# Optimization experiments

Hardware: AMD Instinct MI355X
Metric: run time of the kernel (lower is better)

Reference implementation:

```python
import jax, jax.numpy as jnp
import numpy as np

B, T, D, H, O = 64, 2048, 256, 256, 256


def setup_inputs() -> dict:
    key = jax.random.key(0)
    ks = jax.random.split(key, 4)
    s_d = float(1.0 / np.sqrt(D))
    s_h = float(1.0 / np.sqrt(H))
    return {
        "x": jax.random.normal(ks[0], (B, T, D), jnp.float32),
        "c0": jnp.zeros((B, H), jnp.float32),
        "h0": jnp.zeros((B, H), jnp.float32),
        "Wih": jax.random.normal(ks[1], (D, 4 * H), jnp.float32) * s_d,
        "Whh": jax.random.normal(ks[2], (H, 4 * H), jnp.float32) * s_h,
        "bh": jnp.zeros((4 * H,), jnp.float32),
        "Wout": jax.random.normal(ks[3], (H, O), jnp.float32) * s_h,
        "bout": jnp.zeros((O,), jnp.float32),
    }


def reference(x, c0, h0, Wih, Whh, bh, Wout, bout):
    # Teacher-forcing OneToManyRNN: LSTM cell + Dense projection each step.
    # Gate order (flax LSTMCell): i, f, g, o.
    def step(carry, xt):
        c, h = carry
        gates = xt @ Wih + h @ Whh + bh  # [B, 4H]
        i, f, g, o = jnp.split(gates, 4, axis=-1)
        i = jax.nn.sigmoid(i)
        f = jax.nn.sigmoid(f)
        g = jnp.tanh(g)
        o = jax.nn.sigmoid(o)
        c_new = f * c + i * g
        h_new = o * jnp.tanh(c_new)
        y = h_new @ Wout + bout  # dense_out projection
        return (c_new, h_new), y

    xs = jnp.swapaxes(x, 0, 1)  # [T, B, D]
    _, ys = jax.lax.scan(step, (c0, h0), xs)
    return jnp.swapaxes(ys, 0, 1)  # [B, T, O] (stacked per-step outputs)
```

## Files before the change

kernel.cpp:

```cpp
#include <hip/hip_runtime.h>
#include <hip/hip_fp16.h>
#include <cstdint>
#include <cstddef>

typedef _Float16 half_t;
typedef _Float16 half2_t __attribute__((ext_vector_type(2)));
typedef _Float16 half8_t __attribute__((ext_vector_type(8)));
typedef float    f32x4   __attribute__((ext_vector_type(4)));

#define T_FULL  2048
#define T_CH    512
#define N_CHUNK 4
#define B_SZ    64
#define H_SZ    256
#define G4      1024
#define CH_M    (B_SZ * T_CH)

#define KP_RF   48
#define KP_LDS  7
#define KP_STR  9

static constexpr size_t OFF_XW   = 0;
static constexpr size_t OFF_H    = OFF_XW   + (size_t)CH_M * G4 * 2;
static constexpr size_t OFF_WIH  = OFF_H    + (size_t)CH_M * H_SZ * 2;
static constexpr size_t OFF_WOUT = OFF_WIH  + (size_t)G4 * 256 * 2;
static constexpr size_t OFF_WRF  = OFF_WOUT + (size_t)256 * 256 * 2;
static constexpr size_t OFF_WLDS = OFF_WRF  + (size_t)2 * KP_RF * 1024 * 4;
static constexpr size_t OFF_WSTR = OFF_WLDS + (size_t)2 * KP_LDS * 256 * 16;
static constexpr size_t OFF_SC   = OFF_WSTR + (size_t)2 * KP_STR * 256 * 16;
static constexpr size_t OFF_SH   = OFF_SC   + (size_t)B_SZ * H_SZ * 4;

__device__ __forceinline__ unsigned int packh2(float a, float b) {
    half2_t h; h.x = (half_t)a; h.y = (half_t)b;
    return __builtin_bit_cast(unsigned int, h);
}

__device__ __forceinline__ float dot2f(unsigned int hp, unsigned int wp, float acc) {
#if __has_builtin(__builtin_amdgcn_fdot2)
    return __builtin_amdgcn_fdot2(__builtin_bit_cast(half2_t, hp),
                                  __builtin_bit_cast(half2_t, wp), acc, false);
#else
    half2_t h = __builtin_bit_cast(half2_t, hp);
    half2_t w = __builtin_bit_cast(half2_t, wp);
    return fmaf((float)h.y, (float)w.y, fmaf((float)h.x, (float)w.x, acc));
#endif
}

__device__ __forceinline__ unsigned int rlane(unsigned int v, int lane) {
    return (unsigned int)__builtin_amdgcn_readlane((int)v, lane);
}

__device__ __forceinline__ float sigm(float x)  { return 1.0f / (1.0f + __expf(-x)); }
__device__ __forceinline__ float tanh_(float x) { return 1.0f - 2.0f / (__expf(2.0f * x) + 1.0f); }

static constexpr int PACK_TOTAL = 262144 + 65536 + 2 * KP_RF * 1024
                                + 2 * KP_LDS * 256 * 4 + 2 * KP_STR * 256 * 4
                                + 16384 + 8192;

__global__ __launch_bounds__(256) void pack_kernel(
    const float* __restrict__ Wih, const float* __restrict__ Whh,
    const float* __restrict__ Wout, const float* __restrict__ c0,
    const float* __restrict__ h0,
    half_t* __restrict__ wih_t, half_t* __restrict__ wout_t,
    unsigned int* __restrict__ whh_rf, unsigned int* __restrict__ whh_lds,
    unsigned int* __restrict__ whh_str,
    float* __restrict__ state_c, unsigned int* __restrict__ state_h)
{
    const int stride = gridDim.x * blockDim.x;
    for (int idx = blockIdx.x * blockDim.x + threadIdx.x; idx < PACK_TOTAL; idx += stride) {
        int r = idx;
        if (r < 262144) {
            int n = r >> 8, k = r & 255;
            wih_t[r] = (half_t)Wih[k * 1024 + n];
            continue;
        }
        r -= 262144;
        if (r < 65536) {
            int n = r >> 8, k = r & 255;
            wout_t[r] = (half_t)Wout[k * 256 + n];
            continue;
        }
        r -= 65536;
        if (r < 2 * KP_RF * 1024) {
            int col = r & 1023, q2 = r >> 10;
            int hh = q2 / KP_RF, pl = q2 % KP_RF;
            int k0 = 2 * (hh * 64 + pl);
            whh_rf[r] = packh2(Whh[k0 * 1024 + col], Whh[(k0 + 1) * 1024 + col]);
            continue;
        }
        r -= 2 * KP_RF * 1024;
        if (r < 2 * KP_LDS * 256 * 4) {
            int j = r & 3, e = (r >> 2) & 255, rest = r >> 10;
            int ql = rest % KP_LDS, hh = rest / KP_LDS;
            int k0 = 2 * (hh * 64 + KP_RF + ql);
            int col = j * 256 + e;
            whh_lds[r] = packh2(Whh[k0 * 1024 + col], Whh[(k0 + 1) * 1024 + col]);
            continue;
        }
        r -= 2 * KP_LDS * 256 * 4;
        if (r < 2 * KP_STR * 256 * 4) {
            int j = r & 3, e = (r >> 2) & 255, rest = r >> 10;
            int sl = rest % KP_STR, hh = rest / KP_STR;
            int k0 = 2 * (hh * 64 + KP_RF + KP_LDS + sl);
            int col = j * 256 + e;
            whh_str[r] = packh2(Whh[k0 * 1024 + col], Whh[(k0 + 1) * 1024 + col]);
            continue;
        }
        r -= 2 * KP_STR * 256 * 4;
        if (r < 16384) { state_c[r] = c0[r]; continue; }
        r -= 16384;
        state_h[r] = packh2(h0[2 * r], h0[2 * r + 1]);
    }
}

template<int AMODE, int CMODE>
__global__ __launch_bounds__(256) void gemm16(
    const void* __restrict__ Ap, const half_t* __restrict__ Bt,
    void* __restrict__ Cp, const float* __restrict__ bias, int chunk0)
{
    __shared__ half_t Als[128][40];
    __shared__ half_t Bls[128][40];
    const int tid  = threadIdx.x;
    const int lane = tid & 63, wid = tid >> 6;
    const int wr = wid >> 1, wc = wid & 1;
    const int m0 = blockIdx.x * 128, n0 = blockIdx.y * 128;

    f32x4 acc[4][4] = {};

    for (int kc = 0; kc < 8; ++kc) {
        __syncthreads();
        if (AMODE == 1) {
            const float* A = (const float*)Ap;
            #pragma unroll
            for (int i = 0; i < 4; ++i) {
                int l = tid + i * 256;
                int row = l >> 3, kq = l & 7;
                int m = m0 + row;
                int arow = ((m >> 9) << 11) + chunk0 + (m & 511);
                f32x4 v = *(const f32x4*)(A + (size_t)arow * 256 + kc * 32 + kq * 4);
                uint2 pk;
                pk.x = packh2(v.x, v.y);
                pk.y = packh2(v.z, v.w);
                *reinterpret_cast<uint2*>(&Als[row][kq * 4]) = pk;
            }
        } else {
            const half_t* A = (const half_t*)Ap;
            #pragma unroll
            for (int i = 0; i < 2; ++i) {
                int l = tid + i * 256;
                int row = l >> 2, ko = l & 3;
                half8_t v = *(const half8_t*)(A + (size_t)(m0 + row) * 256 + kc * 32 + ko * 8);
                *reinterpret_cast<half8_t*>(&Als[row][ko * 8]) = v;
            }
        }
        #pragma unroll
        for (int i = 0; i < 2; ++i) {
            int l = tid + i * 256;
            int row = l >> 2, ko = l & 3;
            half8_t v = *(const half8_t*)(Bt + (size_t)(n0 + row) * 256 + kc * 32 + ko * 8);
            *reinterpret_cast<half8_t*>(&Bls[row][ko * 8]) = v;
        }
        __syncthreads();

        half8_t af[4], bf[4];
        #pragma unroll
        for (int mi = 0; mi < 4; ++mi)
            af[mi] = *reinterpret_cast<const half8_t*>(&Als[wr * 64 + mi * 16 + (lane & 15)][(lane >> 4) * 8]);
        #pragma unroll
        for (int ni = 0; ni < 4; ++ni)
            bf[ni] = *reinterpret_cast<const half8_t*>(&Bls[wc * 64 + ni * 16 + (lane & 15)][(lane >> 4) * 8]);
        #pragma unroll
        for (int mi = 0; mi < 4; ++mi)
            #pragma unroll
            for (int ni = 0; ni < 4; ++ni)
                acc[mi][ni] = __builtin_amdgcn_mfma_f32_16x16x32_f16(af[mi], bf[ni], acc[mi][ni], 0, 0, 0);
    }

    #pragma unroll
    for (int mi = 0; mi < 4; ++mi) {
        #pragma unroll
        for (int ni = 0; ni < 4; ++ni) {
            #pragma unroll
            for (int reg = 0; reg < 4; ++reg) {
                int row = m0 + wr * 64 + mi * 16 + (lane >> 4) * 4 + reg;
                int col = n0 + wc * 64 + ni * 16 + (lane & 15);
                float v = acc[mi][ni][reg] + bias[col];
                if (CMODE == 0) {
                    ((half_t*)Cp)[(size_t)row * 1024 + ((col & 255) << 2) + (col >> 8)] = (half_t)v;
                } else {
                    int crow = ((row >> 9) << 11) + chunk0 + (row & 511);
                    ((float*)Cp)[(size_t)crow * 256 + col] = v;
                }
            }
        }
    }
}

__global__ __launch_bounds__(512, 2) void rnn_kernel(
    const unsigned int* __restrict__ whh_rf,
    const uint4* __restrict__ whh_lds,
    const uint4* __restrict__ whh_str,
    const half_t* __restrict__ xw,
    half_t* __restrict__ h_out,
    float* __restrict__ state_c,
    unsigned int* __restrict__ state_h)
{
    __shared__ uint4  lds_w[2 * KP_LDS * 256];
    __shared__ float4 gbuf[256];
    __shared__ unsigned int hbuf[128];

    const int t    = threadIdx.x;
    const int e    = t & 255;
    const int hh   = t >> 8;
    const int lane = t & 63;
    const int b    = blockIdx.x;

    for (int i = t; i < 2 * KP_LDS * 256; i += 512) lds_w[i] = whh_lds[i];
    if (t < 128) hbuf[t] = state_h[b * 128 + t];
    float c = (hh == 0) ? state_c[b * 256 + e] : 0.0f;

    unsigned int wreg[KP_RF][4];
    {
        const unsigned int* wrp = whh_rf + hh * (KP_RF * 1024) + e;
        #pragma unroll
        for (int pl = 0; pl < KP_RF; ++pl)
            #pragma unroll
            for (int j = 0; j < 4; ++j)
                wreg[pl][j] = wrp[pl * 1024 + j * 256];
    }
    __syncthreads();

    const half_t* xwp = xw + (size_t)b * T_CH * 1024 + e * 4;
    half_t* hop = h_out + (size_t)b * T_CH * 256 + e;
    const uint4* strp = whh_str + hh * (KP_STR * 256) + e;
    const uint4* ldp  = lds_w + hh * (KP_LDS * 256) + e;

    for (int step = 0; step < T_CH; ++step) {
        unsigned int hv = hbuf[hh * 64 + lane];

        uint2 xv = {0, 0};
        if (hh == 0) xv = *(const uint2*)xwp;
        uint4 sq[KP_STR];
        #pragma unroll
        for (int sl = 0; sl < KP_STR; ++sl) sq[sl] = strp[sl * 256];

        float a0 = 0.f, a1 = 0.f, a2 = 0.f, a3 = 0.f;

        #pragma unroll
        for (int pl = 0; pl < KP_RF; ++pl) {
            unsigned int s = rlane(hv, pl);
            a0 = dot2f(s, wreg[pl][0], a0);
            a1 = dot2f(s, wreg[pl][1], a1);
            a2 = dot2f(s, wreg[pl][2], a2);
            a3 = dot2f(s, wreg[pl][3], a3);
        }
        #pragma unroll
        for (int sl = 0; sl < KP_STR; ++sl) {
            unsigned int s = rlane(hv, KP_RF + KP_LDS + sl);
            a0 = dot2f(s, sq[sl].x, a0);
            a1 = dot2f(s, sq[sl].y, a1);
            a2 = dot2f(s, sq[sl].z, a2);
            a3 = dot2f(s, sq[sl].w, a3);
        }
        #pragma unroll
        for (int ql = 0; ql < KP_LDS; ++ql) {
            uint4 q = ldp[ql * 256];
            unsigned int s = rlane(hv, KP_RF + ql);
            a0 = dot2f(s, q.x, a0);
            a1 = dot2f(s, q.y, a1);
            a2 = dot2f(s, q.z, a2);
            a3 = dot2f(s, q.w, a3);
        }

        if (hh) {
            float4 p; p.x = a0; p.y = a1; p.z = a2; p.w = a3;
            gbuf[e] = p;
        }
        __syncthreads();

        if (hh == 0) {
            float4 p = gbuf[e];
            half2_t x0 = __builtin_bit_cast(half2_t, xv.x);
            half2_t x1 = __builtin_bit_cast(half2_t, xv.y);
            a0 += p.x + (float)x0.x;
            a1 += p.y + (float)x0.y;
            a2 += p.z + (float)x1.x;
            a3 += p.w + (float)x1.y;
            float ig = sigm(a0), fg = sigm(a1), gg = tanh_(a2), og = sigm(a3);
            c = fg * c + ig * gg;
            float hn = og * tanh_(c);
            half_t h16 = (half_t)hn;
            reinterpret_cast<half_t*>(hbuf)[e] = h16;
            *hop = h16;
        }
        xwp += 1024;
        hop += 256;
        __syncthreads();
    }

    if (hh == 0) state_c[b * 256 + e] = c;
    if (t < 128) state_h[b * 128 + t] = hbuf[t];
}

extern "C" void kernel_launch(void* const* d_in, const int* in_sizes, int n_in,
                              void* d_out, int out_size, void* d_ws, size_t ws_size,
                              hipStream_t stream) {
    const float* x    = (const float*)d_in[0];
    const float* c0   = (const float*)d_in[1];
    const float* h0   = (const float*)d_in[2];
    const float* Wih  = (const float*)d_in[3];
    const float* Whh  = (const float*)d_in[4];
    const float* bh   = (const float*)d_in[5];
    const float* Wout = (const float*)d_in[6];
    const float* bout = (const float*)d_in[7];

    char* ws = (char*)d_ws;
    half_t* xw             = (half_t*)(ws + OFF_XW);
    half_t* h_chunk        = (half_t*)(ws + OFF_H);
    half_t* wih_t          = (half_t*)(ws + OFF_WIH);
    half_t* wout_t         = (half_t*)(ws + OFF_WOUT);
    unsigned int* whh_rf   = (unsigned int*)(ws + OFF_WRF);
    unsigned int* whh_lds  = (unsigned int*)(ws + OFF_WLDS);
    unsigned int* whh_str  = (unsigned int*)(ws + OFF_WSTR);
    float* state_c         = (float*)(ws + OFF_SC);
    unsigned int* state_h  = (unsigned int*)(ws + OFF_SH);

    pack_kernel<<<512, 256, 0, stream>>>(Wih, Whh, Wout, c0, h0,
                                         wih_t, wout_t, whh_rf, whh_lds, whh_str,
                                         state_c, state_h);

    for (int ch = 0; ch < N_CHUNK; ++ch) {
        int chunk0 = ch * T_CH;
        gemm16<1, 0><<<dim3(CH_M / 128, G4 / 128), 256, 0, stream>>>(
            (const void*)x, wih_t, (void*)xw, bh, chunk0);
        rnn_kernel<<<B_SZ, 512, 0, stream>>>(whh_rf, (const uint4*)whh_lds,
                                             (const uint4*)whh_str, xw, h_chunk,
                                             state_c, state_h);
        gemm16<0, 1><<<dim3(CH_M / 128, H_SZ / 128), 256, 0, stream>>>(
            (const void*)h_chunk, wout_t, d_out, bout, chunk0);
    }
    (void)in_sizes; (void)n_in; (void)out_size; (void)ws_size;
}
```

Measured before the change: 4.088 ms.

## Drop streamed global Whh slice; move rows into registers and LDS

Removes the per-step global-memory stream of recurrent weights (9 k-pairs per thread) and redistributes those rows: register-resident slices grow to 50 k-pairs and the LDS slice doubles to 14. Launch bounds drop to one block per SM so the larger register file budget fits, and the h-vector read from LDS is moved to right after the barrier. The aim is to take L2/global latency off the serial recurrence critical path, at the cost of higher register pressure and possible spills.

```diff
diff --git a/kernel.cpp b/kernel.cpp
--- a/kernel.cpp
+++ b/kernel.cpp
@@ -16,9 +16,8 @@
 #define G4      1024
 #define CH_M    (B_SZ * T_CH)
 
-#define KP_RF   48
-#define KP_LDS  7
-#define KP_STR  9
+#define KP_RF   50
+#define KP_LDS  14
 
 static constexpr size_t OFF_XW   = 0;
 static constexpr size_t OFF_H    = OFF_XW   + (size_t)CH_M * G4 * 2;
@@ -26,8 +25,7 @@
 static constexpr size_t OFF_WOUT = OFF_WIH  + (size_t)G4 * 256 * 2;
 static constexpr size_t OFF_WRF  = OFF_WOUT + (size_t)256 * 256 * 2;
 static constexpr size_t OFF_WLDS = OFF_WRF  + (size_t)2 * KP_RF * 1024 * 4;
-static constexpr size_t OFF_WSTR = OFF_WLDS + (size_t)2 * KP_LDS * 256 * 16;
-static constexpr size_t OFF_SC   = OFF_WSTR + (size_t)2 * KP_STR * 256 * 16;
+static constexpr size_t OFF_SC   = OFF_WLDS + (size_t)2 * KP_LDS * 256 * 16;
 static constexpr size_t OFF_SH   = OFF_SC   + (size_t)B_SZ * H_SZ * 4;
 
 __device__ __forceinline__ unsigned int packh2(float a, float b) {
@@ -54,8 +52,7 @@
 __device__ __forceinline__ float tanh_(float x) { return 1.0f - 2.0f / (__expf(2.0f * x) + 1.0f); }
 
 static constexpr int PACK_TOTAL = 262144 + 65536 + 2 * KP_RF * 1024
-                                + 2 * KP_LDS * 256 * 4 + 2 * KP_STR * 256 * 4
-                                + 16384 + 8192;
+                                + 2 * KP_LDS * 256 * 4 + 16384 + 8192;
 
 __global__ __launch_bounds__(256) void pack_kernel(
     const float* __restrict__ Wih, const float* __restrict__ Whh,
@@ -63,7 +60,6 @@
     const float* __restrict__ h0,
     half_t* __restrict__ wih_t, half_t* __restrict__ wout_t,
     unsigned int* __restrict__ whh_rf, unsigned int* __restrict__ whh_lds,
-    unsigned int* __restrict__ whh_str,
     float* __restrict__ state_c, unsigned int* __restrict__ state_h)
 {
     const int stride = gridDim.x * blockDim.x;
@@ -98,15 +94,6 @@
             continue;
         }
         r -= 2 * KP_LDS * 256 * 4;
-        if (r < 2 * KP_STR * 256 * 4) {
-            int j = r & 3, e = (r >> 2) & 255, rest = r >> 10;
-            int sl = rest % KP_STR, hh = rest / KP_STR;
-            int k0 = 2 * (hh * 64 + KP_RF + KP_LDS + sl);
-            int col = j * 256 + e;
-            whh_str[r] = packh2(Whh[k0 * 1024 + col], Whh[(k0 + 1) * 1024 + col]);
-            continue;
-        }
-        r -= 2 * KP_STR * 256 * 4;
         if (r < 16384) { state_c[r] = c0[r]; continue; }
         r -= 16384;
         state_h[r] = packh2(h0[2 * r], h0[2 * r + 1]);
@@ -196,10 +183,9 @@
     }
 }
 
-__global__ __launch_bounds__(512, 2) void rnn_kernel(
+__global__ __launch_bounds__(512, 1) void rnn_kernel(
     const unsigned int* __restrict__ whh_rf,
     const uint4* __restrict__ whh_lds,
-    const uint4* __restrict__ whh_str,
     const half_t* __restrict__ xw,
     half_t* __restrict__ h_out,
     float* __restrict__ state_c,
@@ -232,17 +218,13 @@
 
     const half_t* xwp = xw + (size_t)b * T_CH * 1024 + e * 4;
     half_t* hop = h_out + (size_t)b * T_CH * 256 + e;
-    const uint4* strp = whh_str + hh * (KP_STR * 256) + e;
     const uint4* ldp  = lds_w + hh * (KP_LDS * 256) + e;
 
+    unsigned int hv = hbuf[hh * 64 + lane];
+
     for (int step = 0; step < T_CH; ++step) {
-        unsigned int hv = hbuf[hh * 64 + lane];
-
         uint2 xv = {0, 0};
         if (hh == 0) xv = *(const uint2*)xwp;
-        uint4 sq[KP_STR];
-        #pragma unroll
-        for (int sl = 0; sl < KP_STR; ++sl) sq[sl] = strp[sl * 256];
 
         float a0 = 0.f, a1 = 0.f, a2 = 0.f, a3 = 0.f;
 
@@ -253,14 +235,6 @@
             a1 = dot2f(s, wreg[pl][1], a1);
             a2 = dot2f(s, wreg[pl][2], a2);
             a3 = dot2f(s, wreg[pl][3], a3);
-        }
-        #pragma unroll
-        for (int sl = 0; sl < KP_STR; ++sl) {
-            unsigned int s = rlane(hv, KP_RF + KP_LDS + sl);
-            a0 = dot2f(s, sq[sl].x, a0);
-            a1 = dot2f(s, sq[sl].y, a1);
-            a2 = dot2f(s, sq[sl].z, a2);
-            a3 = dot2f(s, sq[sl].w, a3);
         }
         #pragma unroll
         for (int ql = 0; ql < KP_LDS; ++ql) {
@@ -296,6 +270,7 @@
         xwp += 1024;
         hop += 256;
         __syncthreads();
+        hv = hbuf[hh * 64 + lane];
     }
 
     if (hh == 0) state_c[b * 256 + e] = c;
@@ -321,12 +296,11 @@
     half_t* wout_t         = (half_t*)(ws + OFF_WOUT);
     unsigned int* whh_rf   = (unsigned int*)(ws + OFF_WRF);
     unsigned int* whh_lds  = (unsigned int*)(ws + OFF_WLDS);
-    unsigned int* whh_str  = (unsigned int*)(ws + OFF_WSTR);
     float* state_c         = (float*)(ws + OFF_SC);
     unsigned int* state_h  = (unsigned int*)(ws + OFF_SH);
 
     pack_kernel<<<512, 256, 0, stream>>>(Wih, Whh, Wout, c0, h0,
-                                         wih_t, wout_t, whh_rf, whh_lds, whh_str,
+                                         wih_t, wout_t, whh_rf, whh_lds,
                                          state_c, state_h);
 
     for (int ch = 0; ch < N_CHUNK; ++ch) {
@@ -334,8 +308,7 @@
         gemm16<1, 0><<<dim3(CH_M / 128, G4 / 128), 256, 0, stream>>>(
             (const void*)x, wih_t, (void*)xw, bh, chunk0);
         rnn_kernel<<<B_SZ, 512, 0, stream>>>(whh_rf, (const uint4*)whh_lds,
-                                             (const uint4*)whh_str, xw, h_chunk,
-                                             state_c, state_h);
+                                             xw, h_chunk, state_c, state_h);
         gemm16<0, 1><<<dim3(CH_M / 128, H_SZ / 128), 256, 0, stream>>>(
             (const void*)h_chunk, wout_t, d_out, bout, chunk0);
     }
```

After: 4.234 ms. 3.6% more time.
